# Kernel tuning notes

Measured on AMD Instinct MI355X. Metric: run time of the kernel, lower is better.

Reference implementation:

```python
import jax, jax.numpy as jnp
import numpy as np

N = 100000   # nodes
E = 1600000  # edges (avg degree 16)
F_IN, H1, H2, H3, C = 500, 200, 100, 40, 3


def setup_inputs() -> dict:
    key = jax.random.key(0)
    ks = jax.random.split(key, 10)
    def w(k, shape, fan_in):
        return jax.random.normal(k, shape, dtype=jnp.float32) / np.sqrt(fan_in)
    return {
        "x": jax.random.normal(ks[0], (N, F_IN), dtype=jnp.float32),
        "edge_index": jax.random.randint(ks[1], (2, E), 0, N, dtype=jnp.int32),
        "W1": w(ks[2], (H1, F_IN), F_IN), "b1": jnp.zeros((H1,), jnp.float32),
        "W1b": w(ks[3], (H2, H1), H1),  "b1b": jnp.zeros((H2,), jnp.float32),
        "W2b": w(ks[4], (H3, H2), H2),  "b2b": jnp.zeros((H3,), jnp.float32),
        "W2": w(ks[5], (C, H3), H3),    "b2": jnp.zeros((C,), jnp.float32),
    }


def _gcn_conv(x, W, b, src, dst, norm_e, n):
    # GCNConv: linear transform, then normalized scatter-add aggregation, then bias
    h = x @ W.T                                   # [N, out]
    msgs = h[src] * norm_e[:, None]               # [E+N, out] gathered, normalized
    out = jax.ops.segment_sum(msgs, dst, num_segments=n)
    return out + b


def reference(x, edge_index, W1, b1, W1b, b1b, W2b, b2b, W2, b2):
    n = x.shape[0]
    loop = jnp.arange(n, dtype=edge_index.dtype)
    src = jnp.concatenate([edge_index[0], loop])  # add self-loops (GCNConv default)
    dst = jnp.concatenate([edge_index[1], loop])
    # symmetric normalization: deg computed on target nodes, norm = d^-1/2[src]*d^-1/2[dst]
    deg = jax.ops.segment_sum(jnp.ones_like(dst, dtype=x.dtype), dst, num_segments=n)
    dinv = jnp.where(deg > 0, jax.lax.rsqrt(deg), 0.0)
    norm_e = dinv[src] * dinv[dst]

    # dropout(p=0.5, training=self.training) is identity at inference
    h = jax.nn.relu(_gcn_conv(x, W1, b1, src, dst, norm_e, n))
    h = jax.nn.relu(_gcn_conv(h, W1b, b1b, src, dst, norm_e, n))
    h = jax.nn.relu(_gcn_conv(h, W2b, b2b, src, dst, norm_e, n))
    return _gcn_conv(h, W2, b2, src, dst, norm_e, n)
```

## Files before the change

kernel.cpp:

```cpp
#include <hip/hip_runtime.h>


#define DEV __device__ __forceinline__

typedef __attribute__((ext_vector_type(8))) short short8;
typedef __attribute__((ext_vector_type(4))) float f32x4;
typedef __attribute__((ext_vector_type(4))) _Float16 f16x4;

DEV unsigned short f2bf(float x) {
    unsigned u = __builtin_bit_cast(unsigned, x);
    u += 0x7FFFu + ((u >> 16) & 1u);
    return (unsigned short)(u >> 16);
}
DEV float bf2f(unsigned short b) {
    return __builtin_bit_cast(float, (unsigned)b << 16);
}


__global__ void k_init(int* __restrict__ cnt, int* __restrict__ fill, int n) {
    int i = blockIdx.x * 256 + threadIdx.x;
    if (i < n) { cnt[i] = 1; fill[i] = 0; }
}

__global__ void k_count(const int* __restrict__ dst, int* __restrict__ cnt, int E) {
    int e = blockIdx.x * 256 + threadIdx.x;
    if (e < E) atomicAdd(&cnt[dst[e]], 1);
}

__global__ void k_scan1(const int* __restrict__ cnt, int* __restrict__ row_start,
                        int* __restrict__ partial, float* __restrict__ dinv, int n) {
    __shared__ int sdata[256];
    int base = blockIdx.x * 1024;
    int t = threadIdx.x;
    int v[4]; int sum = 0;
#pragma unroll
    for (int j = 0; j < 4; ++j) {
        int idx = base + t * 4 + j;
        v[j] = (idx < n) ? cnt[idx] : 0;
        if (idx < n) dinv[idx] = rsqrtf((float)v[j]);
        sum += v[j];
    }
    sdata[t] = sum;
    __syncthreads();
    for (int off = 1; off < 256; off <<= 1) {
        int x = (t >= off) ? sdata[t - off] : 0;
        __syncthreads();
        sdata[t] += x;
        __syncthreads();
    }
    int excl = sdata[t] - sum;
#pragma unroll
    for (int j = 0; j < 4; ++j) {
        int idx = base + t * 4 + j;
        if (idx < n) row_start[idx] = excl;
        excl += v[j];
    }
    if (t == 255) partial[blockIdx.x] = sdata[255];
}

__global__ void k_scan2(int* __restrict__ partial, int nb) {
    __shared__ int s[128];
    int t = threadIdx.x;
    int v = (t < nb) ? partial[t] : 0;
    s[t] = v;
    __syncthreads();
    for (int off = 1; off < 128; off <<= 1) {
        int x = (t >= off) ? s[t - off] : 0;
        __syncthreads();
        s[t] += x;
        __syncthreads();
    }
    if (t < nb) partial[t] = s[t] - v;
}

__global__ void k_scan3(int* __restrict__ row_start, const int* __restrict__ partial,
                        int n, int total) {
    int i = blockIdx.x * 256 + threadIdx.x;
    if (i < n) row_start[i] += partial[i >> 10];
    if (i == 0) row_start[n] = total;
}

__global__ void k_fill(const int* __restrict__ src, const int* __restrict__ dst,
                       const int* __restrict__ row_start, int* __restrict__ fill,
                       int* __restrict__ csr_src, int E, int n) {
    int i = blockIdx.x * 256 + threadIdx.x;
    int total = E + n;
    if (i >= total) return;
    int s, d;
    if (i < E) { s = src[i]; d = dst[i]; }
    else       { s = d = i - E; }
    int pos = row_start[d] + atomicAdd(&fill[d], 1);
    csr_src[pos] = s;
}


__global__ void k_wdec(const float* __restrict__ W, int N, int K,
                       unsigned short* __restrict__ Wh, unsigned short* __restrict__ Wl,
                       int NPAD, int KPAD) {
    int i = blockIdx.x * 256 + threadIdx.x;
    if (i >= NPAD * KPAD) return;
    int r = i / KPAD, k = i - r * KPAD;
    float x = (r < N && k < K) ? W[r * K + k] : 0.f;
    unsigned short h = f2bf(x);
    unsigned short l = f2bf(x - bf2f(h));
    Wh[i] = h; Wl[i] = l;
}


template <int NF, typename AT>
__global__ __launch_bounds__(512)
void gemm_mfma(const AT* __restrict__ A, int lda, int M, int K,
               const unsigned short* __restrict__ Wh,
               const unsigned short* __restrict__ Wl, int ldw,
               const float* __restrict__ dinv,
               _Float16* __restrict__ H16, int ldh, int Nout) {
    constexpr int NPAD = NF * 16;
    constexpr int RB = 80;
    __shared__ char lds[2 * NPAD * RB];
    char* ldsH = lds;
    char* ldsL = lds + NPAD * RB;

    const int tid  = threadIdx.x;
    const int wv   = tid >> 6;
    const int lane = tid & 63;
    const int lr   = lane & 15;
    const int kq   = lane >> 4;
    const int m0   = blockIdx.x * 128;

    int arow = m0 + wv * 16 + lr;
    if (arow >= M) arow = M - 1;
    const AT* Arow = A + (size_t)arow * lda;

    f32x4 acc[NF];
#pragma unroll
    for (int f = 0; f < NF; ++f) acc[f] = (f32x4){0.f, 0.f, 0.f, 0.f};

    const int nsteps = (K + 31) / 32;
    for (int s = 0; s < nsteps; ++s) {
        const int kb = s * 32;
        {
            const int CH = NPAD * 4;
            for (int c = tid; c < 2 * CH; c += 512) {
                int b    = (c >= CH);
                int cc   = c - b * CH;
                int r    = cc >> 2;
                int slot = cc & 3;
                const unsigned short* sp = (b ? Wl : Wh) + (size_t)r * ldw + kb + slot * 8;
                uint4 v = *(const uint4*)sp;
                *(uint4*)((b ? ldsL : ldsH) + r * RB + slot * 16) = v;
            }
        }
        __syncthreads();

        float av[8];
        if (kb + 32 <= K) {
            if constexpr (sizeof(AT) == 4) {
                const float* ap = (const float*)Arow + kb + kq * 8;
                f32x4 v0 = *(const f32x4*)ap;
                f32x4 v1 = *(const f32x4*)(ap + 4);
#pragma unroll
                for (int i = 0; i < 4; ++i) { av[i] = v0[i]; av[4 + i] = v1[i]; }
            } else {
                const _Float16* ap = (const _Float16*)Arow + kb + kq * 8;
                f16x4 v0 = *(const f16x4*)ap;
                f16x4 v1 = *(const f16x4*)(ap + 4);
#pragma unroll
                for (int i = 0; i < 4; ++i) { av[i] = (float)v0[i]; av[4 + i] = (float)v1[i]; }
            }
        } else {
#pragma unroll
            for (int i = 0; i < 8; ++i) {
                int k = kb + kq * 8 + i;
                av[i] = (k < K) ? (float)Arow[k] : 0.f;
            }
        }
        short8 ahi, alo;
#pragma unroll
        for (int i = 0; i < 8; ++i) {
            unsigned short h = f2bf(av[i]);
            ahi[i] = (short)h;
            alo[i] = (short)f2bf(av[i] - bf2f(h));
        }

        const int ro = lr * RB + kq * 16;
#pragma unroll
        for (int f = 0; f < NF; ++f) {
            short8 bh = *(const short8*)(ldsH + f * 16 * RB + ro);
            short8 bl = *(const short8*)(ldsL + f * 16 * RB + ro);
            acc[f] = __builtin_amdgcn_mfma_f32_16x16x32_bf16(ahi, bh, acc[f], 0, 0, 0);
            acc[f] = __builtin_amdgcn_mfma_f32_16x16x32_bf16(ahi, bl, acc[f], 0, 0, 0);
            acc[f] = __builtin_amdgcn_mfma_f32_16x16x32_bf16(alo, bh, acc[f], 0, 0, 0);
        }
        __syncthreads();
    }

    const int rbase = m0 + wv * 16 + kq * 4;
    float dv[4];
#pragma unroll
    for (int j = 0; j < 4; ++j) {
        int row = rbase + j;
        dv[j] = (row < M) ? dinv[row] : 0.f;
    }
#pragma unroll
    for (int f = 0; f < NF; ++f) {
        int col = f * 16 + lr;
        if (col >= Nout) continue;
#pragma unroll
        for (int j = 0; j < 4; ++j) {
            int row = rbase + j;
            if (row < M) H16[(size_t)row * ldh + col] = (_Float16)(acc[f][j] * dv[j]);
        }
    }
}


template <int F, bool RELU>
__global__ __launch_bounds__(256)
void agg_f16(const _Float16* __restrict__ h, const int* __restrict__ row_start,
             const int* __restrict__ csr_src, const float* __restrict__ dinv,
             const float* __restrict__ bias, _Float16* __restrict__ out, int n) {
    constexpr int LPN = F / 4;
    constexpr int NPW = 64 / LPN;
    int wave = blockIdx.x * 4 + (threadIdx.x >> 6);
    int lane = threadIdx.x & 63;
    int sub  = lane / LPN;
    int fi   = lane - sub * LPN;
    int node = wave * NPW + sub;
    if (sub >= NPW || node >= n) return;
    int f = fi * 4;
    const _Float16* hf = h + f;

    f32x4 acc = {0.f, 0.f, 0.f, 0.f};
    int e0 = row_start[node], e1 = row_start[node + 1];
    int e = e0;
    for (; e + 4 <= e1; e += 4) {
        int s0 = csr_src[e + 0];
        int s1 = csr_src[e + 1];
        int s2 = csr_src[e + 2];
        int s3 = csr_src[e + 3];
        f16x4 v0 = *(const f16x4*)&hf[(size_t)s0 * F];
        f16x4 v1 = *(const f16x4*)&hf[(size_t)s1 * F];
        f16x4 v2 = *(const f16x4*)&hf[(size_t)s2 * F];
        f16x4 v3 = *(const f16x4*)&hf[(size_t)s3 * F];
        acc += __builtin_convertvector(v0, f32x4);
        acc += __builtin_convertvector(v1, f32x4);
        acc += __builtin_convertvector(v2, f32x4);
        acc += __builtin_convertvector(v3, f32x4);
    }
    for (; e < e1; ++e) {
        int s = csr_src[e];
        f16x4 v = *(const f16x4*)&hf[(size_t)s * F];
        acc += __builtin_convertvector(v, f32x4);
    }
    float dn = dinv[node];
    f32x4 b4 = *(const f32x4*)&bias[f];
    acc = acc * dn + b4;
    if (RELU) {
#pragma unroll
        for (int j = 0; j < 4; ++j) acc[j] = fmaxf(acc[j], 0.f);
    }
    f16x4 o;
#pragma unroll
    for (int j = 0; j < 4; ++j) o[j] = (_Float16)acc[j];
    *(f16x4*)&out[(size_t)node * F + f] = o;
}


__global__ void gemm_small(const _Float16* __restrict__ A, const float* __restrict__ B,
                           const float* __restrict__ dinv, float* __restrict__ C,
                           int M, int K) {
    int m = blockIdx.x * 256 + threadIdx.x;
    if (m >= M) return;
    float a0 = 0.f, a1 = 0.f, a2 = 0.f;
    for (int k = 0; k < K; ++k) {
        float a = (float)A[(size_t)m * K + k];
        a0 += a * B[0 * K + k];
        a1 += a * B[1 * K + k];
        a2 += a * B[2 * K + k];
    }
    float dv = dinv[m];
    C[(size_t)m * 3 + 0] = a0 * dv;
    C[(size_t)m * 3 + 1] = a1 * dv;
    C[(size_t)m * 3 + 2] = a2 * dv;
}

__global__ void agg_f3(const float* __restrict__ h, const int* __restrict__ row_start,
                       const int* __restrict__ csr_src, const float* __restrict__ dinv,
                       const float* __restrict__ bias, float* __restrict__ out, int n) {
    int i = blockIdx.x * 256 + threadIdx.x;
    if (i >= n * 3) return;
    int node = i / 3;
    int f = i - node * 3;
    float acc = 0.f;
    int e1 = row_start[node + 1];
    for (int e = row_start[node]; e < e1; ++e) {
        int s = csr_src[e];
        acc += h[(size_t)s * 3 + f];
    }
    out[i] = acc * dinv[node] + bias[f];
}


extern "C" void kernel_launch(void* const* d_in, const int* in_sizes, int n_in,
                              void* d_out, int out_size, void* d_ws, size_t ws_size,
                              hipStream_t stream) {
    const float* x   = (const float*)d_in[0];
    const int*   ei  = (const int*)d_in[1];
    const float* W1  = (const float*)d_in[2];
    const float* b1  = (const float*)d_in[3];
    const float* W1b = (const float*)d_in[4];
    const float* b1b = (const float*)d_in[5];
    const float* W2b = (const float*)d_in[6];
    const float* b2b = (const float*)d_in[7];
    const float* W2  = (const float*)d_in[8];
    const float* b2  = (const float*)d_in[9];
    float* out = (float*)d_out;

    const int F_IN = 500, H1 = 200, H2 = 100, H3 = 40;
    const int N = in_sizes[0] / F_IN;
    const int E = in_sizes[1] / 2;
    const int* src = ei;
    const int* dst = ei + E;

    size_t off = 0;
    auto alloc = [&](size_t bytes) -> void* {
        void* p = (char*)d_ws + off;
        off += (bytes + 255) & ~(size_t)255;
        return p;
    };
    int*   cnt       = (int*)  alloc((size_t)N * 4);
    int*   row_start = (int*)  alloc((size_t)(N + 1) * 4);
    int*   fill      = (int*)  alloc((size_t)N * 4);
    int*   partial   = (int*)  alloc(128 * 4);
    float* dinv      = (float*)alloc((size_t)N * 4);
    int*   csr_src   = (int*)  alloc((size_t)(E + N) * 4);
    unsigned short* wh1 = (unsigned short*)alloc(208 * 512 * 2);
    unsigned short* wl1 = (unsigned short*)alloc(208 * 512 * 2);
    unsigned short* wh2 = (unsigned short*)alloc(112 * 224 * 2);
    unsigned short* wl2 = (unsigned short*)alloc(112 * 224 * 2);
    unsigned short* wh3 = (unsigned short*)alloc(48 * 128 * 2);
    unsigned short* wl3 = (unsigned short*)alloc(48 * 128 * 2);
    _Float16* h16   = (_Float16*)alloc((size_t)N * H1 * 2);
    _Float16* act16 = (_Float16*)alloc((size_t)N * H1 * 2);
    float*    bufC  = (float*)   alloc((size_t)N * 3 * 4);

    int gN  = (N + 255) / 256;
    int gE  = (E + 255) / 256;
    int gEN = (E + N + 255) / 256;
    int nb  = (N + 1023) / 1024;

    k_init <<<gN, 256, 0, stream>>>(cnt, fill, N);
    k_count<<<gE, 256, 0, stream>>>(dst, cnt, E);
    k_scan1<<<nb, 256, 0, stream>>>(cnt, row_start, partial, dinv, N);
    k_scan2<<<1, 128, 0, stream>>>(partial, nb);
    k_scan3<<<gN, 256, 0, stream>>>(row_start, partial, N, E + N);
    k_fill <<<gEN, 256, 0, stream>>>(src, dst, row_start, fill, csr_src, E, N);

    k_wdec<<<(208 * 512 + 255) / 256, 256, 0, stream>>>(W1,  H1, F_IN, wh1, wl1, 208, 512);
    k_wdec<<<(112 * 224 + 255) / 256, 256, 0, stream>>>(W1b, H2, H1,   wh2, wl2, 112, 224);
    k_wdec<<<( 48 * 128 + 255) / 256, 256, 0, stream>>>(W2b, H3, H2,   wh3, wl3,  48, 128);

    const int gG = (N + 127) / 128;

    gemm_mfma<13, float><<<gG, 512, 0, stream>>>(x, F_IN, N, F_IN, wh1, wl1, 512,
                                                 dinv, h16, H1, H1);
    agg_f16<200, true><<<(N + 3) / 4, 256, 0, stream>>>(h16, row_start, csr_src, dinv,
                                                        b1, act16, N);
    gemm_mfma<7, _Float16><<<gG, 512, 0, stream>>>(act16, H1, N, H1, wh2, wl2, 224,
                                                   dinv, h16, H2, H2);
    agg_f16<100, true><<<(N / 2 + 3) / 4, 256, 0, stream>>>(h16, row_start, csr_src, dinv,
                                                            b1b, act16, N);
    gemm_mfma<3, _Float16><<<gG, 512, 0, stream>>>(act16, H2, N, H2, wh3, wl3, 128,
                                                   dinv, h16, H3, H3);
    {
        int waves = (N + 5) / 6, blocks = (waves + 3) / 4;
        agg_f16<40, true><<<blocks, 256, 0, stream>>>(h16, row_start, csr_src, dinv,
                                                      b2b, act16, N);
    }
    gemm_small<<<(N + 255) / 256, 256, 0, stream>>>(act16, W2, dinv, bufC, N, H3);
    agg_f3<<<(N * 3 + 255) / 256, 256, 0, stream>>>(bufC, row_start, csr_src, dinv,
                                                    b2, out, N);
}
```

Before: 598.2 us.

## Double-buffer weight tiles in LDS and prefetch next K-step in GEMM

Restructures the MFMA GEMM main loop into a two-stage software pipeline. The weight tiles and A fragments for the next K-step are loaded into registers while the current step computes, then written to an alternate LDS buffer, which removes one barrier per step. It also adds a min-blocks hint to the launch bounds. In exchange, LDS use doubles and register pressure rises, which can lower occupancy or cause spills.

```diff
diff --git a/kernel.cpp b/kernel.cpp
--- a/kernel.cpp
+++ b/kernel.cpp
@@ -108,17 +108,19 @@
 
 
 template <int NF, typename AT>
-__global__ __launch_bounds__(512)
+__global__ __launch_bounds__(512, 4)
 void gemm_mfma(const AT* __restrict__ A, int lda, int M, int K,
                const unsigned short* __restrict__ Wh,
                const unsigned short* __restrict__ Wl, int ldw,
                const float* __restrict__ dinv,
                _Float16* __restrict__ H16, int ldh, int Nout) {
     constexpr int NPAD = NF * 16;
-    constexpr int RB = 80;
-    __shared__ char lds[2 * NPAD * RB];
-    char* ldsH = lds;
-    char* ldsL = lds + NPAD * RB;
+    constexpr int RB   = 80;
+    constexpr int BUF  = NPAD * RB;
+    constexpr int CH   = NPAD * 4;
+    constexpr int CH2  = 2 * CH;
+    constexpr int NW   = (CH2 + 511) / 512;
+    __shared__ char lds[4 * BUF];
 
     const int tid  = threadIdx.x;
     const int wv   = tid >> 6;
@@ -136,32 +138,46 @@
     for (int f = 0; f < NF; ++f) acc[f] = (f32x4){0.f, 0.f, 0.f, 0.f};
 
     const int nsteps = (K + 31) / 32;
-    for (int s = 0; s < nsteps; ++s) {
+
+    auto loadW = [&](int s, uint4* w) {
         const int kb = s * 32;
-        {
-            const int CH = NPAD * 4;
-            for (int c = tid; c < 2 * CH; c += 512) {
+#pragma unroll
+        for (int j = 0; j < NW; ++j) {
+            int c = tid + j * 512;
+            if (c < CH2) {
                 int b    = (c >= CH);
                 int cc   = c - b * CH;
                 int r    = cc >> 2;
                 int slot = cc & 3;
-                const unsigned short* sp = (b ? Wl : Wh) + (size_t)r * ldw + kb + slot * 8;
-                uint4 v = *(const uint4*)sp;
-                *(uint4*)((b ? ldsL : ldsH) + r * RB + slot * 16) = v;
+                w[j] = *(const uint4*)((b ? Wl : Wh) + (size_t)r * ldw + kb + slot * 8);
             }
         }
-        __syncthreads();
-
+    };
+    auto writeW = [&](char* base, const uint4* w) {
+#pragma unroll
+        for (int j = 0; j < NW; ++j) {
+            int c = tid + j * 512;
+            if (c < CH2) {
+                int b    = (c >= CH);
+                int cc   = c - b * CH;
+                int r    = cc >> 2;
+                int slot = cc & 3;
+                *(uint4*)(base + b * BUF + r * RB + slot * 16) = w[j];
+            }
+        }
+    };
+    auto loadA = [&](int s, short8& ahi, short8& alo) {
+        const int kb = s * 32 + kq * 8;
         float av[8];
-        if (kb + 32 <= K) {
+        if (kb + 8 <= K) {
             if constexpr (sizeof(AT) == 4) {
-                const float* ap = (const float*)Arow + kb + kq * 8;
+                const float* ap = (const float*)Arow + kb;
                 f32x4 v0 = *(const f32x4*)ap;
                 f32x4 v1 = *(const f32x4*)(ap + 4);
 #pragma unroll
                 for (int i = 0; i < 4; ++i) { av[i] = v0[i]; av[4 + i] = v1[i]; }
             } else {
-                const _Float16* ap = (const _Float16*)Arow + kb + kq * 8;
+                const _Float16* ap = (const _Float16*)Arow + kb;
                 f16x4 v0 = *(const f16x4*)ap;
                 f16x4 v1 = *(const f16x4*)(ap + 4);
 #pragma unroll
@@ -170,27 +186,49 @@
         } else {
 #pragma unroll
             for (int i = 0; i < 8; ++i) {
-                int k = kb + kq * 8 + i;
+                int k = kb + i;
                 av[i] = (k < K) ? (float)Arow[k] : 0.f;
             }
         }
-        short8 ahi, alo;
 #pragma unroll
         for (int i = 0; i < 8; ++i) {
             unsigned short h = f2bf(av[i]);
             ahi[i] = (short)h;
             alo[i] = (short)f2bf(av[i] - bf2f(h));
         }
-
+    };
+    auto compute = [&](const char* base, const short8& ahi, const short8& alo) {
         const int ro = lr * RB + kq * 16;
 #pragma unroll
         for (int f = 0; f < NF; ++f) {
-            short8 bh = *(const short8*)(ldsH + f * 16 * RB + ro);
-            short8 bl = *(const short8*)(ldsL + f * 16 * RB + ro);
+            short8 bh = *(const short8*)(base + f * 16 * RB + ro);
+            short8 bl = *(const short8*)(base + BUF + f * 16 * RB + ro);
             acc[f] = __builtin_amdgcn_mfma_f32_16x16x32_bf16(ahi, bh, acc[f], 0, 0, 0);
             acc[f] = __builtin_amdgcn_mfma_f32_16x16x32_bf16(ahi, bl, acc[f], 0, 0, 0);
             acc[f] = __builtin_amdgcn_mfma_f32_16x16x32_bf16(alo, bh, acc[f], 0, 0, 0);
         }
+    };
+
+    uint4 wA[NW], wB[NW];
+    short8 aAh, aAl, aBh, aBl;
+
+    loadW(0, wA);
+    loadA(0, aAh, aAl);
+    writeW(lds, wA);
+    __syncthreads();
+
+    for (int s = 0; s < nsteps; s += 2) {
+        const bool p1 = (s + 1 < nsteps);
+        if (p1) { loadW(s + 1, wB); loadA(s + 1, aBh, aBl); }
+        compute(lds, aAh, aAl);
+        if (p1) writeW(lds + 2 * BUF, wB);
+        __syncthreads();
+        if (!p1) break;
+
+        const bool p2 = (s + 2 < nsteps);
+        if (p2) { loadW(s + 2, wA); loadA(s + 2, aAh, aAl); }
+        compute(lds + 2 * BUF, aBh, aBl);
+        if (p2) writeW(lds, wA);
         __syncthreads();
     }
 
```

New measurement: 835.4 us. +39.6%, slower.

## Double-buffer weight tiles in LDS and prefetch A/W for next k-step

Applied to the files above, without the earlier changes.

Restructures the MFMA GEMM main loop to use two LDS buffers. Next-step weight chunks and A fragments are loaded into registers while the current step's MFMAs run, then stored to the alternate buffer, which leaves one barrier per step. The LDS row stride changes from padded 80 bytes to 64 bytes with an XOR swizzle to avoid bank conflicts. This doubles LDS usage and adds register pressure for the prefetched values, which may cut occupancy.

```diff
diff --git a/kernel.cpp b/kernel.cpp
--- a/kernel.cpp
+++ b/kernel.cpp
@@ -107,6 +107,8 @@
 }
 
 
+struct A8 { f32x4 lo, hi; };
+
 template <int NF, typename AT>
 __global__ __launch_bounds__(512)
 void gemm_mfma(const AT* __restrict__ A, int lda, int M, int K,
@@ -115,10 +117,12 @@
                const float* __restrict__ dinv,
                _Float16* __restrict__ H16, int ldh, int Nout) {
     constexpr int NPAD = NF * 16;
-    constexpr int RB = 80;
-    __shared__ char lds[2 * NPAD * RB];
-    char* ldsH = lds;
-    char* ldsL = lds + NPAD * RB;
+    constexpr int HBUF = NPAD * 64;
+    constexpr int BUFB = 2 * HBUF;
+    constexpr int CH   = NPAD * 4;
+    constexpr int CH2  = 2 * CH;
+    constexpr int NW   = (CH2 + 511) / 512;
+    __shared__ char lds[2 * BUFB];
 
     const int tid  = threadIdx.x;
     const int wv   = tid >> 6;
@@ -131,49 +135,84 @@
     if (arow >= M) arow = M - 1;
     const AT* Arow = A + (size_t)arow * lda;
 
-    f32x4 acc[NF];
-#pragma unroll
-    for (int f = 0; f < NF; ++f) acc[f] = (f32x4){0.f, 0.f, 0.f, 0.f};
-
-    const int nsteps = (K + 31) / 32;
-    for (int s = 0; s < nsteps; ++s) {
-        const int kb = s * 32;
-        {
-            const int CH = NPAD * 4;
-            for (int c = tid; c < 2 * CH; c += 512) {
-                int b    = (c >= CH);
-                int cc   = c - b * CH;
-                int r    = cc >> 2;
-                int slot = cc & 3;
-                const unsigned short* sp = (b ? Wl : Wh) + (size_t)r * ldw + kb + slot * 8;
-                uint4 v = *(const uint4*)sp;
-                *(uint4*)((b ? ldsL : ldsH) + r * RB + slot * 16) = v;
-            }
-        }
-        __syncthreads();
-
-        float av[8];
-        if (kb + 32 <= K) {
+    const unsigned short* wgp[NW];
+    int  wlo[NW];
+    bool wok[NW];
+#pragma unroll
+    for (int j = 0; j < NW; ++j) {
+        int c  = tid + j * 512;
+        wok[j] = (c < CH2);
+        int cw = wok[j] ? c : 0;
+        int b  = (cw >= CH) ? 1 : 0;
+        int cc = cw - b * CH;
+        int r  = cc >> 2;
+        int sl = cc & 3;
+        int gs = sl ^ (r & 3);
+        wgp[j] = (b ? Wl : Wh) + (size_t)r * ldw + gs * 8;
+        wlo[j] = b * HBUF + r * 64 + sl * 16;
+    }
+
+    auto loadA = [&](int s) -> A8 {
+        A8 o;
+        int kb = s * 32 + kq * 8;
+        if (kb + 8 <= K) {
             if constexpr (sizeof(AT) == 4) {
-                const float* ap = (const float*)Arow + kb + kq * 8;
-                f32x4 v0 = *(const f32x4*)ap;
-                f32x4 v1 = *(const f32x4*)(ap + 4);
-#pragma unroll
-                for (int i = 0; i < 4; ++i) { av[i] = v0[i]; av[4 + i] = v1[i]; }
+                const float* ap = (const float*)Arow + kb;
+                o.lo = *(const f32x4*)ap;
+                o.hi = *(const f32x4*)(ap + 4);
             } else {
-                const _Float16* ap = (const _Float16*)Arow + kb + kq * 8;
+                const _Float16* ap = (const _Float16*)Arow + kb;
                 f16x4 v0 = *(const f16x4*)ap;
                 f16x4 v1 = *(const f16x4*)(ap + 4);
-#pragma unroll
-                for (int i = 0; i < 4; ++i) { av[i] = (float)v0[i]; av[4 + i] = (float)v1[i]; }
+                o.lo = __builtin_convertvector(v0, f32x4);
+                o.hi = __builtin_convertvector(v1, f32x4);
             }
         } else {
 #pragma unroll
-            for (int i = 0; i < 8; ++i) {
-                int k = kb + kq * 8 + i;
-                av[i] = (k < K) ? (float)Arow[k] : 0.f;
+            for (int i = 0; i < 4; ++i) {
+                int k0 = kb + i, k1 = kb + 4 + i;
+                o.lo[i] = (k0 < K) ? (float)Arow[k0] : 0.f;
+                o.hi[i] = (k1 < K) ? (float)Arow[k1] : 0.f;
             }
         }
+        return o;
+    };
+
+    f32x4 acc[NF];
+#pragma unroll
+    for (int f = 0; f < NF; ++f) acc[f] = (f32x4){0.f, 0.f, 0.f, 0.f};
+
+    const int nsteps = (K + 31) / 32;
+    uint4 wreg[NW];
+
+#pragma unroll
+    for (int j = 0; j < NW; ++j)
+        if (wok[j]) wreg[j] = *(const uint4*)(wgp[j]);
+    A8 acur = loadA(0);
+#pragma unroll
+    for (int j = 0; j < NW; ++j)
+        if (wok[j]) *(uint4*)(lds + wlo[j]) = wreg[j];
+    __syncthreads();
+
+    const int ro = lr * 64 + ((kq ^ (lr & 3)) << 4);
+
+    for (int s = 0; s < nsteps; ++s) {
+        const char* bb = lds + (s & 1) * BUFB;
+        char*       bn = lds + ((s + 1) & 1) * BUFB;
+        const bool more = (s + 1 < nsteps);
+
+        if (more) {
+#pragma unroll
+            for (int j = 0; j < NW; ++j)
+                if (wok[j]) wreg[j] = *(const uint4*)(wgp[j] + (size_t)(s + 1) * 32);
+        }
+        A8 anxt;
+        if (more) anxt = loadA(s + 1);
+        else      { anxt.lo = (f32x4){0,0,0,0}; anxt.hi = (f32x4){0,0,0,0}; }
+
+        float av[8];
+#pragma unroll
+        for (int i = 0; i < 4; ++i) { av[i] = acur.lo[i]; av[4 + i] = acur.hi[i]; }
         short8 ahi, alo;
 #pragma unroll
         for (int i = 0; i < 8; ++i) {
@@ -182,16 +221,22 @@
             alo[i] = (short)f2bf(av[i] - bf2f(h));
         }
 
-        const int ro = lr * RB + kq * 16;
 #pragma unroll
         for (int f = 0; f < NF; ++f) {
-            short8 bh = *(const short8*)(ldsH + f * 16 * RB + ro);
-            short8 bl = *(const short8*)(ldsL + f * 16 * RB + ro);
+            short8 bh = *(const short8*)(bb + f * 1024 + ro);
+            short8 bl = *(const short8*)(bb + HBUF + f * 1024 + ro);
             acc[f] = __builtin_amdgcn_mfma_f32_16x16x32_bf16(ahi, bh, acc[f], 0, 0, 0);
             acc[f] = __builtin_amdgcn_mfma_f32_16x16x32_bf16(ahi, bl, acc[f], 0, 0, 0);
             acc[f] = __builtin_amdgcn_mfma_f32_16x16x32_bf16(alo, bh, acc[f], 0, 0, 0);
         }
+
+        if (more) {
+#pragma unroll
+            for (int j = 0; j < NW; ++j)
+                if (wok[j]) *(uint4*)(bn + wlo[j]) = wreg[j];
+        }
         __syncthreads();
+        acur = anxt;
     }
 
     const int rbase = m0 + wv * 16 + kq * 4;
```

After: 695.5 us. 16.3% more time.
